# Kernel tuning notes

Hardware: AMD Instinct MI355X
Metric: run time of the kernel (lower is better)

Reference implementation:

```python
import jax, jax.numpy as jnp
import numpy as np

B, N, I_IN, O_OUT, S_EX, S_PHI, S_RHO = 1024, 32, 6, 5, 10, 60, 60
N_ACTIONS, N_ROLES = 5, 7


def _gru(x, h, Wih, Whh, bih, bhh):
    # PyTorch GRUCell math
    gi = x @ Wih.T + bih
    gh = h @ Whh.T + bhh
    ir, iz, inn = jnp.split(gi, 3, axis=-1)
    hr, hz, hn = jnp.split(gh, 3, axis=-1)
    r = jax.nn.sigmoid(ir + hr)
    u = jax.nn.sigmoid(iz + hz)
    n = jnp.tanh(inn + r * hn)
    return (1.0 - u) * n + u * h


def setup_inputs():
    key = jax.random.key(0)
    ks = jax.random.split(key, 32)
    has = (jax.random.uniform(ks[0], (B, N)) < 0.8).astype(jnp.float32)  # per-batch node existence
    z = jax.random.normal(ks[1], (B, N, S_EX), jnp.float32)
    dz = jax.random.normal(ks[2], (B, N, S_EX), jnp.float32)
    # union-graph DAG adjacency: adj[j, i] == edge j -> i, j < i (strictly upper triangular)
    adj = jnp.triu(jax.random.uniform(ks[3], (N, N)) < 0.3, k=1)

    def U(k, shape, fan_in):
        s = 1.0 / np.sqrt(fan_in)
        return jax.random.uniform(k, shape, jnp.float32, -s, s)

    fin = S_PHI + 2 * S_EX
    p = {
        'Wih_f': U(ks[4], (3 * S_PHI, S_RHO), S_PHI),
        'Whh_f': U(ks[5], (3 * S_PHI, S_PHI), S_PHI),
        'bih_f': U(ks[6], (3 * S_PHI,), S_PHI),
        'bhh_f': U(ks[7], (3 * S_PHI,), S_PHI),
        'Wih_b': U(ks[8], (3 * S_PHI, S_RHO), S_PHI),
        'Whh_b': U(ks[9], (3 * S_PHI, S_PHI), S_PHI),
        'bih_b': U(ks[10], (3 * S_PHI,), S_PHI),
        'bhh_b': U(ks[11], (3 * S_PHI,), S_PHI),
        'Wf': U(ks[12], (S_RHO, fin), fin), 'bf': U(ks[13], (S_RHO,), fin),
        'Wb': U(ks[14], (S_RHO, fin), fin), 'bb': U(ks[15], (S_RHO,), fin),
        'Wa': U(ks[16], (N_ACTIONS, 2 * S_PHI), 2 * S_PHI), 'ba': U(ks[17], (N_ACTIONS,), 2 * S_PHI),
        'Wc': U(ks[18], (1, 2 * S_PHI), 2 * S_PHI), 'bc': U(ks[19], (1,), 2 * S_PHI),
        'Wu': U(ks[20], (N_ROLES, 2 * S_RHO), 2 * S_RHO), 'bu': U(ks[21], (N_ROLES,), 2 * S_RHO),
    }
    return {'has': has, 'z': z, 'dz': dz, 'adj': adj, **p}


def reference(has, z, dz, adj,
              Wih_f, Whh_f, bih_f, bhh_f,
              Wih_b, Whh_b, bih_b, bhh_b,
              Wf, bf, Wb, bb, Wa, ba, Wc, bc, Wu, bu):
    adjf = adj.astype(z.dtype)

    # ---- forward message pass over DAG (ascending node order) ----
    def fwd_node(rho_f, i):
        def step(h, j):
            m = adjf[j, i] * has[:, j][:, None]  # interpolate mask: edge exists AND source node exists
            h2 = _gru(rho_f[j], h, Wih_f, Whh_f, bih_f, bhh_f)
            return h + m * (h2 - h), None
        h, _ = jax.lax.scan(step, jnp.zeros((B, S_PHI), z.dtype), jnp.arange(N))
        rho_i = jnp.tanh(jnp.concatenate([h, z[:, i], dz[:, i]], 1) @ Wf.T + bf)
        return rho_f.at[i].set(rho_i), None

    rho_f, _ = jax.lax.scan(fwd_node, jnp.zeros((N, B, S_RHO), z.dtype), jnp.arange(N))

    # ---- backward message pass (descending node order, descending out-neighbors) ----
    def bwd_node(rho_b, i):
        def step(h, j):
            m = adjf[i, j] * has[:, j][:, None]
            h2 = _gru(rho_b[j], h, Wih_b, Whh_b, bih_b, bhh_b)
            return h + m * (h2 - h), None
        h, _ = jax.lax.scan(step, jnp.zeros((B, S_PHI), z.dtype), jnp.arange(N - 1, -1, -1))
        rho_i = jnp.concatenate([h, z[:, i], dz[:, i]], 1) @ Wb.T + bb  # fc_backward has no activation
        return rho_b.at[i].set(rho_i), None

    rho_b, _ = jax.lax.scan(bwd_node, jnp.zeros((N, B, S_RHO), z.dtype), jnp.arange(N - 1, -1, -1))

    # ---- alpha aggregations over output / input nodes ----
    def alpha_f_step(h, i):
        h2 = _gru(rho_f[i], h, Wih_f, Whh_f, bih_f, bhh_f)
        return h + has[:, i][:, None] * (h2 - h), None
    alpha_f, _ = jax.lax.scan(alpha_f_step, jnp.zeros((B, S_RHO), z.dtype), jnp.arange(N - O_OUT, N))

    def alpha_b_step(h, i):
        h2 = _gru(rho_b[i], h, Wih_b, Whh_b, bih_b, bhh_b)
        return h + has[:, i][:, None] * (h2 - h), None
    alpha_b, _ = jax.lax.scan(alpha_b_step, jnp.zeros((B, S_RHO), z.dtype), jnp.arange(I_IN - 1, -1, -1))

    glob = jnp.concatenate([alpha_f, alpha_b], 1)  # [B, 2*S_phi]
    omega = glob @ Wa.T + ba                        # [B, 5]
    value = glob @ Wc.T + bc                        # [B, 1]

    psi = jnp.concatenate([rho_f, rho_b], -1) @ Wu.T + bu  # [N, B, 7]
    psi = jnp.transpose(psi, (1, 2, 0))                    # [B, 7, N]
    mask = has[:, None, :]
    psi = -60.0 * (1.0 - mask) + psi * mask                # interpolate(-60, psi, has)

    instr_prob = jax.nn.softmax(omega, axis=1)
    role_prob = jax.nn.softmax(psi, axis=1)
    return instr_prob, role_prob, value
```

## Files before the change

kernel.cpp:

```cpp
#include <hip/hip_runtime.h>


namespace {

typedef float v2f __attribute__((ext_vector_type(2)));

constexpr int Bc = 1024;
constexpr int Nn = 32;
constexpr int SP = 60;
constexpr int NA = 5;
constexpr int NR = 7;

constexpr int WS_WIH = 24576;
constexpr int WS_WP  = 49152;
constexpr int WS_TOTAL = 59392;
constexpr int DSTRIDE_G = 12288;
constexpr int DSTRIDE_P = 5120;

constexpr int OFF_ST   = 0;
constexpr int OFF_RP   = 4096;
constexpr int OFF_PART = 5120;
constexpr int OFF_ZDZ  = 13312;
constexpr int OFF_PSI  = 14592;
constexpr int OFF_WU   = 15104;
constexpr int OFF_WA   = 15944;
constexpr int OFF_WC   = 16544;
constexpr int OFF_BA   = 16664;
constexpr int OFF_BU   = 16672;
constexpr int OFF_BC   = 16680;
constexpr int OFF_HAS  = 16684;
constexpr int OFF_AF   = 16748;
constexpr int OFF_AB   = 16876;
constexpr int OFF_OS   = 17004;
constexpr int OFF_MASK = 17020;
constexpr int LDS_FLOATS = OFF_MASK + 68 + 8;

__device__ __forceinline__ float sigm(float x) {
    return 1.0f / (1.0f + __expf(-x));
}

__device__ __forceinline__ float tanh_f(float x) {
    float e = __expf(fminf(2.0f * x, 80.0f));
    return (e - 1.0f) / (e + 1.0f);
}

__device__ __forceinline__ unsigned adj_nz(const unsigned* a, int mode, int r, int c) {
    const int idx = r * 32 + c;
    unsigned v = (mode == 1) ? ((a[idx >> 2] >> (8 * (idx & 3))) & 0xffu) : a[idx];
    return v != 0u ? 1u : 0u;
}

__device__ __forceinline__ void matvec3(const v2f (&W)[3][8], const v2f* x,
                                        float& r0, float& r1, float& r2) {
    v2f a0 = {0.f, 0.f}, a1 = {0.f, 0.f}, a2 = {0.f, 0.f};
#pragma unroll
    for (int p = 0; p < 8; ++p) {
        const v2f xp = x[p];
        a0 = __builtin_elementwise_fma(W[0][p], xp, a0);
        a1 = __builtin_elementwise_fma(W[1][p], xp, a1);
        a2 = __builtin_elementwise_fma(W[2][p], xp, a2);
    }
    r0 = a0.x + a0.y; r1 = a1.x + a1.y; r2 = a2.x + a2.y;
}

__device__ __forceinline__ void load_w(const float* __restrict__ ws, int d,
        int w, int lane, v2f onev,
        v2f (&wh)[3][8], v2f (&wx)[3][8], v2f (&wp)[10]) {
    const v2f* WH = (const v2f*)(ws + d * DSTRIDE_G + ((lane * 4 + w) << 4));
    const v2f* WX = (const v2f*)(ws + WS_WIH + d * DSTRIDE_G + ((lane * 4 + w) << 4));
    const v2f* WPp = (const v2f*)(ws + WS_WP + d * DSTRIDE_P + (lane * 4 + w) * 20);
#pragma unroll
    for (int g = 0; g < 3; ++g)
#pragma unroll
        for (int p = 0; p < 8; ++p) {
            wh[g][p] = WH[g * 2048 + p] * onev;
            wx[g][p] = WX[g * 2048 + p] * onev;
        }
#pragma unroll
    for (int p = 0; p < 10; ++p) wp[p] = WPp[p] * onev;
}

__global__ void pack_kernel(const float* __restrict__ Whh_f, const float* __restrict__ Wih_f,
                            const float* __restrict__ Wf,
                            const float* __restrict__ Whh_b, const float* __restrict__ Wih_b,
                            const float* __restrict__ Wb, float* __restrict__ ws) {
    const int idx = blockIdx.x * 256 + threadIdx.x;
    if (idx < 2 * 24576) {
        const int which = idx / 24576;
        int r = idx % 24576;
        const int j = r & 15; r >>= 4;
        const int w = r & 3;  r >>= 2;
        const int lane = r & 63; r >>= 6;
        const int g = r % 3;
        const int d = r / 3;
        const int k = 16 * w + j;
        const float* src = which ? (d ? Wih_b : Wih_f) : (d ? Whh_b : Whh_f);
        ws[idx] = (lane < 60 && k < 60) ? src[(g * 60 + lane) * 60 + k] : 0.f;
    } else if (idx < WS_TOTAL) {
        int r = idx - WS_WP;
        const int jj = r % 20; r /= 20;
        const int w = r & 3;  r >>= 2;
        const int lane = r & 63;
        const int d = r >> 6;
        const float* src = d ? Wb : Wf;
        const int pk = (w < 3) ? 20 * w : 60;
        ws[idx] = (lane < 60) ? src[lane * 80 + pk + jj] : 0.f;
    }
}

__device__ __forceinline__ void gru_fin(float* lds, int s, int slot, int lane,
        float b0s, float b1s, float b2i, float b2h,
        float* hrow, float m, bool act) {
    const int base = OFF_PART + ((s * 4 + slot) * 4) * 256;
    const float4 q0 = *(const float4*)(lds + base + (0 * 64 + lane) * 4);
    const float4 q1 = *(const float4*)(lds + base + (1 * 64 + lane) * 4);
    const float4 q2 = *(const float4*)(lds + base + (2 * 64 + lane) * 4);
    const float4 q3 = *(const float4*)(lds + base + (3 * 64 + lane) * 4);
    const float a0  = q0.x + q1.x + q2.x + q3.x + b0s;
    const float a1  = q0.y + q1.y + q2.y + q3.y + b1s;
    const float a2i = q0.z + q1.z + q2.z + q3.z + b2i;
    const float a2h = q0.w + q1.w + q2.w + q3.w + b2h;
    const float r = sigm(a0);
    const float u = sigm(a1);
    const float n = tanh_f(fmaf(r, a2h, a2i));
    const float hold = hrow[lane];
    const float h2 = fmaf(u, hold - n, n);
    const float hnew = fmaf(m, h2 - hold, hold);
    if (act) hrow[lane] = hnew;
}

template <int FWD>
__device__ __forceinline__ void run_dir(float* lds,
        const v2f (&wh)[3][8], const v2f (&wx)[3][8], const v2f (&wp)[10],
        const float* __restrict__ bih, const float* __restrict__ bhh,
        const float* __restrict__ bp, int w, int lane, int ln, int& par) {
    float* st0 = lds + OFF_ST;
    float* st1 = lds + OFF_ST + 2048;
    const unsigned* succm = (const unsigned*)(lds + OFF_MASK);
    const unsigned* predm = succm + 32;
    const bool act = lane < SP;

    const float b0s = bih[ln] + bhh[ln];
    const float b1s = bih[60 + ln] + bhh[60 + ln];
    const float b2i = bih[120 + ln];
    const float b2h = bhh[120 + ln];
    const float bpv = bp[ln];

    for (int s = 0; s < Nn; ++s) {
        const int t = FWD ? s : (Nn - 1 - s);

        v2f pa0 = {0.f, 0.f}, pa1 = {0.f, 0.f};
        const v2f* xb0 = (w < 3) ? ((const v2f*)(st0 + t * 64) + 10 * w)
                                 : ((const v2f*)(lds + OFF_ZDZ + t * 20));
        const v2f* xb1 = (w < 3) ? ((const v2f*)(st1 + t * 64) + 10 * w)
                                 : ((const v2f*)(lds + OFF_ZDZ + 640 + t * 20));
#pragma unroll
        for (int p = 0; p < 10; ++p) {
            pa0 = __builtin_elementwise_fma(wp[p], xb0[p], pa0);
            pa1 = __builtin_elementwise_fma(wp[p], xb1[p], pa1);
        }
        lds[OFF_RP + ((par * 2 + 0) * 4 + w) * 64 + lane] = pa0.x + pa0.y;
        lds[OFF_RP + ((par * 2 + 1) * 4 + w) * 64 + lane] = pa1.x + pa1.y;
        __syncthreads();
        float sum0 = lds[OFF_RP + ((par * 2) * 4 + 0) * 64 + lane]
                   + lds[OFF_RP + ((par * 2) * 4 + 1) * 64 + lane]
                   + lds[OFF_RP + ((par * 2) * 4 + 2) * 64 + lane]
                   + lds[OFF_RP + ((par * 2) * 4 + 3) * 64 + lane] + bpv;
        float sum1 = lds[OFF_RP + ((par * 2 + 1) * 4 + 0) * 64 + lane]
                   + lds[OFF_RP + ((par * 2 + 1) * 4 + 1) * 64 + lane]
                   + lds[OFF_RP + ((par * 2 + 1) * 4 + 2) * 64 + lane]
                   + lds[OFF_RP + ((par * 2 + 1) * 4 + 3) * 64 + lane] + bpv;
        par ^= 1;
        const float rho0 = FWD ? tanh_f(sum0) : sum0;
        const float rho1 = FWD ? tanh_f(sum1) : sum1;
        if (act) { st0[t * 64 + lane] = rho0; st1[t * 64 + lane] = rho1; }

        const float m0 = lds[OFF_HAS + t];
        const float m1 = lds[OFF_HAS + 32 + t];
        unsigned mk = (m0 != 0.f || m1 != 0.f) ? (FWD ? succm[t] : predm[t]) : 0u;
        if (mk) {
            float gA0, gA1, gA2, gB0, gB1, gB2;
            matvec3(wx, (const v2f*)(st0 + t * 64) + 8 * w, gA0, gA1, gA2);
            matvec3(wx, (const v2f*)(st1 + t * 64) + 8 * w, gB0, gB1, gB2);
            while (mk) {
                int i0 = __ffs(mk) - 1; mk &= mk - 1u;
                int i1 = -1, i2 = -1, i3 = -1, cnt = 1;
                if (mk) { i1 = __ffs(mk) - 1; mk &= mk - 1u; ++cnt;
                    if (mk) { i2 = __ffs(mk) - 1; mk &= mk - 1u; ++cnt;
                        if (mk) { i3 = __ffs(mk) - 1; mk &= mk - 1u; ++cnt; } } }
                const int ii[4] = {i0, i1, i2, i3};
#pragma unroll
                for (int j = 0; j < 4; ++j) {
                    if (j >= cnt) break;
                    float g0, g1, g2;
                    matvec3(wh, (const v2f*)(st0 + ii[j] * 64) + 8 * w, g0, g1, g2);
                    float4 q = {gA0 + g0, gA1 + g1, gA2, g2};
                    *(float4*)(lds + OFF_PART + ((0 * 4 + j) * 4 + w) * 256 + lane * 4) = q;
                    matvec3(wh, (const v2f*)(st1 + ii[j] * 64) + 8 * w, g0, g1, g2);
                    float4 q2v = {gB0 + g0, gB1 + g1, gB2, g2};
                    *(float4*)(lds + OFF_PART + ((1 * 4 + j) * 4 + w) * 256 + lane * 4) = q2v;
                }
                __syncthreads();
                if (w < cnt) {
                    const int it = ii[w];
                    gru_fin(lds, 0, w, lane, b0s, b1s, b2i, b2h, st0 + it * 64, m0, act);
                    gru_fin(lds, 1, w, lane, b0s, b1s, b2i, b2h, st1 + it * 64, m1, act);
                }
                __syncthreads();
            }
        }
    }

    float* ah0 = lds + (FWD ? OFF_AF : OFF_AB);
    float* ah1 = ah0 + 64;
    ah0[lane] = 0.f; ah1[lane] = 0.f;
    const int acn = FWD ? 5 : 6;
    for (int s2 = 0; s2 < acn; ++s2) {
        const int i = FWD ? (Nn - 5 + s2) : (5 - s2);
        const float m0 = lds[OFF_HAS + i];
        const float m1 = lds[OFF_HAS + 32 + i];
        if (m0 == 0.f && m1 == 0.f) continue;
        float gA0, gA1, gA2, gB0, gB1, gB2, g0, g1, g2;
        matvec3(wx, (const v2f*)(st0 + i * 64) + 8 * w, gA0, gA1, gA2);
        matvec3(wh, (const v2f*)(ah0) + 8 * w, g0, g1, g2);
        float4 q = {gA0 + g0, gA1 + g1, gA2, g2};
        *(float4*)(lds + OFF_PART + ((0 * 4 + 0) * 4 + w) * 256 + lane * 4) = q;
        matvec3(wx, (const v2f*)(st1 + i * 64) + 8 * w, gB0, gB1, gB2);
        matvec3(wh, (const v2f*)(ah1) + 8 * w, g0, g1, g2);
        float4 q2v = {gB0 + g0, gB1 + g1, gB2, g2};
        *(float4*)(lds + OFF_PART + ((1 * 4 + 0) * 4 + w) * 256 + lane * 4) = q2v;
        __syncthreads();
        if (w == 0)      gru_fin(lds, 0, 0, lane, b0s, b1s, b2i, b2h, ah0, m0, act);
        else if (w == 1) gru_fin(lds, 1, 0, lane, b0s, b1s, b2i, b2h, ah1, m1, act);
        __syncthreads();
    }
}

__device__ void run_heads(float* lds, int s, int b, int lane, float* __restrict__ out) {
    const float* aF = lds + OFF_AF + s * 64;
    const float* aB = lds + OFF_AB + s * 64;

    float o = 0.f;
    if (lane < NA) {
        o = lds[OFF_BA + lane];
        const float* wa = lds + OFF_WA + lane * 120;
#pragma unroll
        for (int k = 0; k < SP; ++k) o = fmaf(wa[k], aF[k], o);
#pragma unroll
        for (int k = 0; k < SP; ++k) o = fmaf(wa[60 + k], aB[k], o);
        lds[OFF_OS + s * 8 + lane] = o;
    } else if (lane == NA) {
        float v = lds[OFF_BC];
        const float* wc = lds + OFF_WC;
#pragma unroll
        for (int k = 0; k < SP; ++k) v = fmaf(wc[k], aF[k], v);
#pragma unroll
        for (int k = 0; k < SP; ++k) v = fmaf(wc[60 + k], aB[k], v);
        out[Bc * NA + Bc * NR * Nn + b] = v;
    }
    __builtin_amdgcn_wave_barrier();

    if (lane < NA) {
        const float* os = lds + OFF_OS + s * 8;
        float mx = os[0];
#pragma unroll
        for (int j = 1; j < NA; ++j) mx = fmaxf(mx, os[j]);
        float sum = 0.f;
#pragma unroll
        for (int j = 0; j < NA; ++j) sum += __expf(os[j] - mx);
        out[b * NA + lane] = __expf(o - mx) / sum;
    }

    if (lane < Nn) {
        const int i = lane;
        const float mkk = lds[OFF_HAS + s * 32 + i];
        float p[NR];
        float mx = -1e30f;
#pragma unroll
        for (int c = 0; c < NR; ++c) {
            const float v = (mkk != 0.f)
                ? (lds[OFF_PSI + s * 256 + i * 8 + c] + lds[OFF_BU + c])
                : -60.0f;
            p[c] = v;
            mx = fmaxf(mx, v);
        }
        float sum = 0.f;
#pragma unroll
        for (int c = 0; c < NR; ++c) { p[c] = __expf(p[c] - mx); sum += p[c]; }
        const float inv = 1.0f / sum;
#pragma unroll
        for (int c = 0; c < NR; ++c)
            out[Bc * NA + b * (NR * Nn) + c * Nn + i] = p[c] * inv;
    }
}

__global__ __launch_bounds__(256, 2)
void dn_kernel(const float* __restrict__ has, const float* __restrict__ z,
               const float* __restrict__ dz, const unsigned* __restrict__ adjw,
               const float* __restrict__ bih_f, const float* __restrict__ bhh_f,
               const float* __restrict__ bih_b, const float* __restrict__ bhh_b,
               const float* __restrict__ bf, const float* __restrict__ bb,
               const float* __restrict__ Wa, const float* __restrict__ ba,
               const float* __restrict__ Wc, const float* __restrict__ bc,
               const float* __restrict__ Wu, const float* __restrict__ bu,
               const float* __restrict__ ws, float* __restrict__ out) {
    __shared__ float lds[LDS_FLOATS];
    const int tid = threadIdx.x;
    const int lane = tid & 63;
    const int w = tid >> 6;
    const int b0 = blockIdx.x * 2;
    const int ln = (lane < SP) ? lane : (SP - 1);

    unsigned* succm = (unsigned*)(lds + OFF_MASK);
    unsigned* predm = succm + 32;
    unsigned* flags = predm + 32;

    if (tid < 4) flags[tid] = 0u;
    __syncthreads();

    {
        unsigned ff = 0u, fb = 0u;
        for (int i = tid; i < 256; i += 256) {
            const unsigned v = adjw[i];
            ff |= (v == 0x3f800000u) ? 1u : 0u;
            fb |= (v > 1u && v != 0x3f800000u) ? 1u : 0u;
        }
        if (ff) atomicOr(&flags[0], 1u);
        if (fb) atomicOr(&flags[1], 1u);
    }

    for (int i = tid; i < 840; i += 256) lds[OFF_WU + i] = Wu[i];
    for (int i = tid; i < 600; i += 256) lds[OFF_WA + i] = Wa[i];
    if (tid < 120) lds[OFF_WC + tid] = Wc[tid];
    if (tid < NR) lds[OFF_BU + tid] = bu[tid];
    if (tid < NA) lds[OFF_BA + tid] = ba[tid];
    if (tid == 0) lds[OFF_BC] = bc[0];
    if (tid < 64) lds[OFF_HAS + tid] = has[(b0 + (tid >> 5)) * 32 + (tid & 31)];
    for (int i = tid; i < 2 * Nn * 20; i += 256) {
        const int ss = i / 640, r = i - ss * 640;
        const int t = r / 20, k = r - t * 20;
        lds[OFF_ZDZ + i] = (k < 10) ? z[((b0 + ss) * Nn + t) * 10 + k]
                                    : dz[((b0 + ss) * Nn + t) * 10 + (k - 10)];
    }
    for (int i = tid; i < 2 * Nn * 64; i += 256) lds[OFF_ST + i] = 0.f;
    __syncthreads();

    const int mode = flags[0] ? 2 : (flags[1] ? 1 : 0);
    if (tid < 32) {
        unsigned sm = 0u;
        for (int c = 0; c < 32; ++c) sm |= adj_nz(adjw, mode, tid, c) << c;
        succm[tid] = sm;
    } else if (tid < 64) {
        const int c = tid - 32;
        unsigned pm = 0u;
        for (int r = 0; r < 32; ++r) pm |= adj_nz(adjw, mode, r, c) << r;
        predm[c] = pm;
    }
    __syncthreads();

    float one = 1.0f;
    asm volatile("" : "+v"(one));
    const v2f onev = {one, one};

    int par = 0;
    v2f wh[3][8], wx[3][8], wp[10];

    load_w(ws, 0, w, lane, onev, wh, wx, wp);
    run_dir<1>(lds, wh, wx, wp, bih_f, bhh_f, bf, w, lane, ln, par);
    __syncthreads();

    if (tid < Nn * NR) {
        const int i = tid / NR, c = tid - i * NR;
        const float* wu = lds + OFF_WU + c * 120;
        const float* s0 = lds + OFF_ST + i * 64;
        const float* s1 = lds + OFF_ST + 2048 + i * 64;
        float a0 = 0.f, a1 = 0.f;
#pragma unroll
        for (int k = 0; k < SP; ++k) {
            a0 = fmaf(wu[k], s0[k], a0);
            a1 = fmaf(wu[k], s1[k], a1);
        }
        lds[OFF_PSI + i * 8 + c] = a0;
        lds[OFF_PSI + 256 + i * 8 + c] = a1;
    }
    __syncthreads();

    for (int i = tid; i < 2 * Nn * 64; i += 256) lds[OFF_ST + i] = 0.f;
    __syncthreads();

    load_w(ws, 1, w, lane, onev, wh, wx, wp);
    run_dir<0>(lds, wh, wx, wp, bih_b, bhh_b, bb, w, lane, ln, par);
    __syncthreads();

    if (tid < Nn * NR) {
        const int i = tid / NR, c = tid - i * NR;
        const float* wu = lds + OFF_WU + c * 120 + 60;
        const float* s0 = lds + OFF_ST + i * 64;
        const float* s1 = lds + OFF_ST + 2048 + i * 64;
        float a0 = 0.f, a1 = 0.f;
#pragma unroll
        for (int k = 0; k < SP; ++k) {
            a0 = fmaf(wu[k], s0[k], a0);
            a1 = fmaf(wu[k], s1[k], a1);
        }
        lds[OFF_PSI + i * 8 + c] += a0;
        lds[OFF_PSI + 256 + i * 8 + c] += a1;
    }
    __syncthreads();

    if (w == 0) run_heads(lds, 0, b0, lane, out);
    else if (w == 1) run_heads(lds, 1, b0 + 1, lane, out);
}

}

extern "C" void kernel_launch(void* const* d_in, const int* in_sizes, int n_in,
                              void* d_out, int out_size, void* d_ws, size_t ws_size,
                              hipStream_t stream) {
    (void)in_sizes; (void)n_in; (void)out_size; (void)ws_size;
    const float* has     = (const float*)d_in[0];
    const float* z       = (const float*)d_in[1];
    const float* dz      = (const float*)d_in[2];
    const unsigned* adjw = (const unsigned*)d_in[3];
    const float* Wih_f   = (const float*)d_in[4];
    const float* Whh_f   = (const float*)d_in[5];
    const float* bih_f   = (const float*)d_in[6];
    const float* bhh_f   = (const float*)d_in[7];
    const float* Wih_b   = (const float*)d_in[8];
    const float* Whh_b   = (const float*)d_in[9];
    const float* bih_b   = (const float*)d_in[10];
    const float* bhh_b   = (const float*)d_in[11];
    const float* Wf      = (const float*)d_in[12];
    const float* bf      = (const float*)d_in[13];
    const float* Wb      = (const float*)d_in[14];
    const float* bb      = (const float*)d_in[15];
    const float* Wa      = (const float*)d_in[16];
    const float* ba      = (const float*)d_in[17];
    const float* Wc      = (const float*)d_in[18];
    const float* bc      = (const float*)d_in[19];
    const float* Wu      = (const float*)d_in[20];
    const float* bu      = (const float*)d_in[21];
    float* out = (float*)d_out;
    float* ws  = (float*)d_ws;

    pack_kernel<<<(WS_TOTAL + 255) / 256, 256, 0, stream>>>(
        Whh_f, Wih_f, Wf, Whh_b, Wih_b, Wb, ws);

    dn_kernel<<<Bc / 2, 256, 0, stream>>>(
        has, z, dz, adjw,
        bih_f, bhh_f, bih_b, bhh_b, bf, bb,
        Wa, ba, Wc, bc, Wu, bu, ws, out);
}
```

Baseline: 345.7 us.

## Batch up to six DAG successor updates per barrier pair and read head weights from global

The message-passing loop now gathers up to six successor/predecessor nodes per round instead of four, so fewer barrier-separated rounds are needed for high-degree nodes. The GRU finalisation work (node × sample) is spread across all four waves in up to three repetitions instead of one wave per node handling both samples. To make room for the larger partial-sum buffer in LDS, the head weights (Wu, Wa, Wc and biases) are no longer staged in LDS and are read directly from global memory. This trades fewer synchronisations and better wave utilisation for more register pressure and uncached-in-LDS global weight reads in the psi and head stages.

After: 340.4 us. Within noise of the previous version (-1.5%).

```diff
diff --git a/kernel.cpp b/kernel.cpp
--- a/kernel.cpp
+++ b/kernel.cpp
@@ -10,6 +10,7 @@
 constexpr int SP = 60;
 constexpr int NA = 5;
 constexpr int NR = 7;
+constexpr int CHK = 6;
 
 constexpr int WS_WIH = 24576;
 constexpr int WS_WP  = 49152;
@@ -20,19 +21,13 @@
 constexpr int OFF_ST   = 0;
 constexpr int OFF_RP   = 4096;
 constexpr int OFF_PART = 5120;
-constexpr int OFF_ZDZ  = 13312;
-constexpr int OFF_PSI  = 14592;
-constexpr int OFF_WU   = 15104;
-constexpr int OFF_WA   = 15944;
-constexpr int OFF_WC   = 16544;
-constexpr int OFF_BA   = 16664;
-constexpr int OFF_BU   = 16672;
-constexpr int OFF_BC   = 16680;
-constexpr int OFF_HAS  = 16684;
-constexpr int OFF_AF   = 16748;
-constexpr int OFF_AB   = 16876;
-constexpr int OFF_OS   = 17004;
-constexpr int OFF_MASK = 17020;
+constexpr int OFF_ZDZ  = 17408;
+constexpr int OFF_PSI  = 18688;
+constexpr int OFF_HAS  = 19200;
+constexpr int OFF_AF   = 19264;
+constexpr int OFF_AB   = 19392;
+constexpr int OFF_OS   = 19520;
+constexpr int OFF_MASK = 19536;
 constexpr int LDS_FLOATS = OFF_MASK + 68 + 8;
 
 __device__ __forceinline__ float sigm(float x) {
@@ -111,7 +106,7 @@
 __device__ __forceinline__ void gru_fin(float* lds, int s, int slot, int lane,
         float b0s, float b1s, float b2i, float b2h,
         float* hrow, float m, bool act) {
-    const int base = OFF_PART + ((s * 4 + slot) * 4) * 256;
+    const int base = OFF_PART + ((s * CHK + slot) * 4) * 256;
     const float4 q0 = *(const float4*)(lds + base + (0 * 64 + lane) * 4);
     const float4 q1 = *(const float4*)(lds + base + (1 * 64 + lane) * 4);
     const float4 q2 = *(const float4*)(lds + base + (2 * 64 + lane) * 4);
@@ -184,27 +179,38 @@
             matvec3(wx, (const v2f*)(st1 + t * 64) + 8 * w, gB0, gB1, gB2);
             while (mk) {
                 int i0 = __ffs(mk) - 1; mk &= mk - 1u;
-                int i1 = -1, i2 = -1, i3 = -1, cnt = 1;
+                int i1 = -1, i2 = -1, i3 = -1, i4 = -1, i5 = -1, cnt = 1;
                 if (mk) { i1 = __ffs(mk) - 1; mk &= mk - 1u; ++cnt;
-                    if (mk) { i2 = __ffs(mk) - 1; mk &= mk - 1u; ++cnt;
-                        if (mk) { i3 = __ffs(mk) - 1; mk &= mk - 1u; ++cnt; } } }
-                const int ii[4] = {i0, i1, i2, i3};
-#pragma unroll
-                for (int j = 0; j < 4; ++j) {
+                 if (mk) { i2 = __ffs(mk) - 1; mk &= mk - 1u; ++cnt;
+                  if (mk) { i3 = __ffs(mk) - 1; mk &= mk - 1u; ++cnt;
+                   if (mk) { i4 = __ffs(mk) - 1; mk &= mk - 1u; ++cnt;
+                    if (mk) { i5 = __ffs(mk) - 1; mk &= mk - 1u; ++cnt; } } } } }
+                const int ii[CHK] = {i0, i1, i2, i3, i4, i5};
+#pragma unroll
+                for (int j = 0; j < CHK; ++j) {
                     if (j >= cnt) break;
                     float g0, g1, g2;
                     matvec3(wh, (const v2f*)(st0 + ii[j] * 64) + 8 * w, g0, g1, g2);
                     float4 q = {gA0 + g0, gA1 + g1, gA2, g2};
-                    *(float4*)(lds + OFF_PART + ((0 * 4 + j) * 4 + w) * 256 + lane * 4) = q;
+                    *(float4*)(lds + OFF_PART + (((0 * CHK + j) * 4 + w) * 64 + lane) * 4) = q;
                     matvec3(wh, (const v2f*)(st1 + ii[j] * 64) + 8 * w, g0, g1, g2);
                     float4 q2v = {gB0 + g0, gB1 + g1, gB2, g2};
-                    *(float4*)(lds + OFF_PART + ((1 * 4 + j) * 4 + w) * 256 + lane * 4) = q2v;
+                    *(float4*)(lds + OFF_PART + (((1 * CHK + j) * 4 + w) * 64 + lane) * 4) = q2v;
                 }
                 __syncthreads();
-                if (w < cnt) {
-                    const int it = ii[w];
-                    gru_fin(lds, 0, w, lane, b0s, b1s, b2i, b2h, st0 + it * 64, m0, act);
-                    gru_fin(lds, 1, w, lane, b0s, b1s, b2i, b2h, st1 + it * 64, m1, act);
+                {
+                    const int nt = cnt * 2;
+#pragma unroll
+                    for (int rep = 0; rep < 3; ++rep) {
+                        const int task = w + rep * 4;
+                        if (task < nt) {
+                            const int sl = task >> 1, sm = task & 1;
+                            const int it = ii[sl];
+                            float* hrow = (sm ? st1 : st0) + it * 64;
+                            gru_fin(lds, sm, sl, lane, b0s, b1s, b2i, b2h,
+                                    hrow, sm ? m1 : m0, act);
+                        }
+                    }
                 }
                 __syncthreads();
             }
@@ -224,11 +230,11 @@
         matvec3(wx, (const v2f*)(st0 + i * 64) + 8 * w, gA0, gA1, gA2);
         matvec3(wh, (const v2f*)(ah0) + 8 * w, g0, g1, g2);
         float4 q = {gA0 + g0, gA1 + g1, gA2, g2};
-        *(float4*)(lds + OFF_PART + ((0 * 4 + 0) * 4 + w) * 256 + lane * 4) = q;
+        *(float4*)(lds + OFF_PART + (((0 * CHK) * 4 + w) * 64 + lane) * 4) = q;
         matvec3(wx, (const v2f*)(st1 + i * 64) + 8 * w, gB0, gB1, gB2);
         matvec3(wh, (const v2f*)(ah1) + 8 * w, g0, g1, g2);
         float4 q2v = {gB0 + g0, gB1 + g1, gB2, g2};
-        *(float4*)(lds + OFF_PART + ((1 * 4 + 0) * 4 + w) * 256 + lane * 4) = q2v;
+        *(float4*)(lds + OFF_PART + (((1 * CHK) * 4 + w) * 64 + lane) * 4) = q2v;
         __syncthreads();
         if (w == 0)      gru_fin(lds, 0, 0, lane, b0s, b1s, b2i, b2h, ah0, m0, act);
         else if (w == 1) gru_fin(lds, 1, 0, lane, b0s, b1s, b2i, b2h, ah1, m1, act);
@@ -236,26 +242,28 @@
     }
 }
 
-__device__ void run_heads(float* lds, int s, int b, int lane, float* __restrict__ out) {
+__device__ void run_heads(float* lds, int s, int b, int lane,
+                          const float* __restrict__ Wa, const float* __restrict__ ba,
+                          const float* __restrict__ Wc, const float* __restrict__ bc,
+                          const float* __restrict__ bu, float* __restrict__ out) {
     const float* aF = lds + OFF_AF + s * 64;
     const float* aB = lds + OFF_AB + s * 64;
 
     float o = 0.f;
     if (lane < NA) {
-        o = lds[OFF_BA + lane];
-        const float* wa = lds + OFF_WA + lane * 120;
+        o = ba[lane];
+        const float* wa = Wa + lane * 120;
 #pragma unroll
         for (int k = 0; k < SP; ++k) o = fmaf(wa[k], aF[k], o);
 #pragma unroll
         for (int k = 0; k < SP; ++k) o = fmaf(wa[60 + k], aB[k], o);
         lds[OFF_OS + s * 8 + lane] = o;
     } else if (lane == NA) {
-        float v = lds[OFF_BC];
-        const float* wc = lds + OFF_WC;
-#pragma unroll
-        for (int k = 0; k < SP; ++k) v = fmaf(wc[k], aF[k], v);
-#pragma unroll
-        for (int k = 0; k < SP; ++k) v = fmaf(wc[60 + k], aB[k], v);
+        float v = bc[0];
+#pragma unroll
+        for (int k = 0; k < SP; ++k) v = fmaf(Wc[k], aF[k], v);
+#pragma unroll
+        for (int k = 0; k < SP; ++k) v = fmaf(Wc[60 + k], aB[k], v);
         out[Bc * NA + Bc * NR * Nn + b] = v;
     }
     __builtin_amdgcn_wave_barrier();
@@ -279,7 +287,7 @@
 #pragma unroll
         for (int c = 0; c < NR; ++c) {
             const float v = (mkk != 0.f)
-                ? (lds[OFF_PSI + s * 256 + i * 8 + c] + lds[OFF_BU + c])
+                ? (lds[OFF_PSI + s * 256 + i * 8 + c] + bu[c])
                 : -60.0f;
             p[c] = v;
             mx = fmaxf(mx, v);
@@ -329,12 +337,6 @@
         if (fb) atomicOr(&flags[1], 1u);
     }
 
-    for (int i = tid; i < 840; i += 256) lds[OFF_WU + i] = Wu[i];
-    for (int i = tid; i < 600; i += 256) lds[OFF_WA + i] = Wa[i];
-    if (tid < 120) lds[OFF_WC + tid] = Wc[tid];
-    if (tid < NR) lds[OFF_BU + tid] = bu[tid];
-    if (tid < NA) lds[OFF_BA + tid] = ba[tid];
-    if (tid == 0) lds[OFF_BC] = bc[0];
     if (tid < 64) lds[OFF_HAS + tid] = has[(b0 + (tid >> 5)) * 32 + (tid & 31)];
     for (int i = tid; i < 2 * Nn * 20; i += 256) {
         const int ss = i / 640, r = i - ss * 640;
@@ -371,7 +373,7 @@
 
     if (tid < Nn * NR) {
         const int i = tid / NR, c = tid - i * NR;
-        const float* wu = lds + OFF_WU + c * 120;
+        const float* wu = Wu + c * 120;
         const float* s0 = lds + OFF_ST + i * 64;
         const float* s1 = lds + OFF_ST + 2048 + i * 64;
         float a0 = 0.f, a1 = 0.f;
@@ -394,7 +396,7 @@
 
     if (tid < Nn * NR) {
         const int i = tid / NR, c = tid - i * NR;
-        const float* wu = lds + OFF_WU + c * 120 + 60;
+        const float* wu = Wu + c * 120 + 60;
         const float* s0 = lds + OFF_ST + i * 64;
         const float* s1 = lds + OFF_ST + 2048 + i * 64;
         float a0 = 0.f, a1 = 0.f;
@@ -408,8 +410,8 @@
     }
     __syncthreads();
 
-    if (w == 0) run_heads(lds, 0, b0, lane, out);
-    else if (w == 1) run_heads(lds, 1, b0 + 1, lane, out);
+    if (w == 0) run_heads(lds, 0, b0, lane, Wa, ba, Wc, bc, bu, out);
+    else if (w == 1) run_heads(lds, 1, b0 + 1, lane, Wa, ba, Wc, bc, bu, out);
 }
 
 }
```
